# Performance work log

Hardware: AMD Instinct MI355X
Metric: run time of the kernel (lower is better)

Reference implementation:

```python
import jax, jax.numpy as jnp
import numpy as np

B, T, H, STEPS = 8192, 128, 128, 30
BN_EPS = 1e-5


def gru_cell(x, h, w_ih, w_hh, b_ih, b_hh):
    # PyTorch GRU gate math: gates ordered (r, z, n)
    gi = x @ w_ih.T + b_ih            # [B, 3H]
    gh = h @ w_hh.T + b_hh            # [B, 3H]
    ir, iz, inn = jnp.split(gi, 3, axis=-1)
    hr, hz, hn = jnp.split(gh, 3, axis=-1)
    r = jax.nn.sigmoid(ir + hr)
    z = jax.nn.sigmoid(iz + hz)
    n = jnp.tanh(inn + r * hn)
    return (1.0 - z) * n + z * h


def setup_inputs() -> dict:
    key = jax.random.key(0)
    ks = jax.random.split(key, 10)
    s = lambda k, shape: jax.random.normal(k, shape, jnp.float32) * 0.05
    z = lambda *shape: jnp.zeros(shape, jnp.float32)
    return {
        "past": jax.random.normal(ks[0], (B, 6, T), jnp.float32),
        "conv_w": s(ks[1], (H, 6, 3)),
        "conv_b": z(H),
        "bn_gamma": jnp.ones((1,), jnp.float32),
        "bn_beta": z(1),
        "bn_mean": z(1),
        "bn_var": jnp.ones((1,), jnp.float32),
        "enc_wih": s(ks[2], (3 * H, H)),
        "enc_whh": s(ks[3], (3 * H, H)),
        "enc_bih": z(3 * H),
        "enc_bhh": z(3 * H),
        "dec_wih": s(ks[4], (3 * H, H)),
        "dec_whh": s(ks[5], (3 * H, H)),
        "dec_bih": z(3 * H),
        "dec_bhh": z(3 * H),
        "fc1_w": s(ks[6], (256, H)),
        "fc1_b": z(256),
        "fc2_w": s(ks[7], (64, 256)),
        "fc2_b": z(64),
        "fc3_w": s(ks[8], (6, 64)),
        "fc3_b": z(6),
    }


def reference(past, conv_w, conv_b, bn_gamma, bn_beta, bn_mean, bn_var,
              enc_wih, enc_whh, enc_bih, enc_bhh,
              dec_wih, dec_whh, dec_bih, dec_bhh,
              fc1_w, fc1_b, fc2_w, fc2_b, fc3_w, fc3_b):
    b = past.shape[0]
    # Conv1d(6 -> 128, k=3, pad=1) + ReLU
    y = jax.lax.conv_general_dilated(
        past, conv_w, window_strides=(1,), padding=[(1, 1)],
        dimension_numbers=("NCH", "OIH", "NCH"))
    y = jax.nn.relu(y + conv_b[None, :, None])
    # BatchNorm2d(1) in eval mode: single-channel affine normalization over whole tensor
    y = bn_gamma[0] * (y - bn_mean[0]) * jax.lax.rsqrt(bn_var[0] + BN_EPS) + bn_beta[0]
    # encoder GRU over time: [B,128,T] -> [T,B,128]
    xs = jnp.transpose(y, (2, 0, 1))
    h0 = jnp.zeros((b, H), y.dtype)

    def enc_step(h, x):
        return gru_cell(x, h, enc_wih, enc_whh, enc_bih, enc_bhh), None

    state_past, _ = jax.lax.scan(enc_step, h0, xs)  # [B,128]

    def mlp(h):
        a = jax.nn.relu(h @ fc1_w.T + fc1_b)
        a = a @ fc2_w.T + fc2_b   # no activation between fc2 and fc3 (matches Sequential)
        return a @ fc3_w.T + fc3_b

    # decoder input is state_past at step 0, zeros afterwards
    dec_inputs = jnp.concatenate(
        [state_past[None], jnp.zeros((STEPS - 1, b, H), y.dtype)], axis=0)
    present0 = past[:, :, -1]  # [B,6]

    def dec_step(carry, x):
        h, present = carry
        h = gru_cell(x, h, dec_wih, dec_whh, dec_bih, dec_bhh)
        present = present + mlp(h)
        return (h, present), present

    _, preds = jax.lax.scan(dec_step, (jnp.zeros((b, H), y.dtype), present0), dec_inputs)
    # preds: [30,B,6] -> [B,6,30] (matches prediction.permute(0,2,1))
    return jnp.transpose(preds, (1, 2, 0))
```

## Files before the change

kernel.cpp:

```cpp
#include <hip/hip_runtime.h>

#define DI __device__ __forceinline__

typedef __attribute__((ext_vector_type(8))) short short8;
typedef __attribute__((ext_vector_type(4))) float f32x4;

constexpr int THREADS = 512;
constexpr int ROWS    = 32;
constexpr int NBLK    = 8192 / ROWS;
constexpr int PITCH   = 272;
constexpr int PITCH2  = 528;
constexpr int SPITCH  = 256;

constexpr int O_STAGE = 0;
constexpr int O_PATCH = 98304;
constexpr int O_XALL  = 108544;
constexpr int O_H     = 143360;
constexpr int HBUF    = 8704;
constexpr int O_FC3W  = 160768;
constexpr int LDS_TOTAL = 162304;
constexpr int O_A1D   = 98304;
constexpr int O_A2D   = 115200;

DI unsigned cvtpk2(float lo, float hi){
  unsigned r;
  asm("v_cvt_pk_bf16_f32 %0, %1, %2" : "=v"(r) : "v"(lo), "v"(hi));
  return r;
}
DI unsigned short f2bf(float f){ return (unsigned short)cvtpk2(f, f); }
DI float bf2f(unsigned short u){
  union { unsigned u; float f; } v; v.u = ((unsigned)u) << 16;
  return v.f;
}
DI float u2f_lo(unsigned u){ union { unsigned u; float f; } v; v.u = u << 16;        return v.f; }
DI float u2f_hi(unsigned u){ union { unsigned u; float f; } v; v.u = u & 0xffff0000u; return v.f; }
DI float sigm(float x){ return __builtin_amdgcn_rcpf(1.f + __expf(-x)); }
DI float tanh_(float x){ return 2.f * __builtin_amdgcn_rcpf(1.f + __expf(-2.f * x)) - 1.f; }
DI f32x4 mfma16(short8 a, short8 b, f32x4 c){
  return __builtin_amdgcn_mfma_f32_16x16x32_bf16(a, b, c, 0, 0, 0);
}
DI uint2 pack4(f32x4 v){
  return make_uint2(cvtpk2(v[0], v[1]), cvtpk2(v[2], v[3]));
}
DI f32x4 unpack4(uint2 u){
  return (f32x4){u2f_lo(u.x), u2f_hi(u.x), u2f_lo(u.y), u2f_hi(u.y)};
}

DI void stage_k128(char* dst, const float* __restrict__ src, int nrows, int tid){
  const int total = nrows * 32;
  for (int i = tid; i < total; i += THREADS){
    float4 v = ((const float4*)src)[i];
    int e = i << 2;
    int n = e >> 7, k = e & 127;
    *(uint2*)(dst + n * SPITCH + k * 2) = make_uint2(cvtpk2(v.x, v.y), cvtpk2(v.z, v.w));
  }
}
DI void stage_k256(char* dst, const float* __restrict__ src, int nrows, int tid){
  const int total = nrows * 64;
  for (int i = tid; i < total; i += THREADS){
    float4 v = ((const float4*)src)[i];
    int e = i << 2;
    int n = e >> 8, k = e & 255;
    *(uint2*)(dst + n * PITCH2 + k * 2) = make_uint2(cvtpk2(v.x, v.y), cvtpk2(v.z, v.w));
  }
}

__global__ void __launch_bounds__(THREADS, 2)
gru_fused(const float* __restrict__ past,
          const float* __restrict__ conv_w, const float* __restrict__ conv_b,
          const float* __restrict__ bn_gamma, const float* __restrict__ bn_beta,
          const float* __restrict__ bn_mean, const float* __restrict__ bn_var,
          const float* __restrict__ enc_wih, const float* __restrict__ enc_whh,
          const float* __restrict__ enc_bih, const float* __restrict__ enc_bhh,
          const float* __restrict__ dec_wih, const float* __restrict__ dec_whh,
          const float* __restrict__ dec_bih, const float* __restrict__ dec_bhh,
          const float* __restrict__ fc1_w, const float* __restrict__ fc1_b,
          const float* __restrict__ fc2_w, const float* __restrict__ fc2_b,
          const float* __restrict__ fc3_w, const float* __restrict__ fc3_b,
          float* __restrict__ out)
{
  extern __shared__ char smem[];
  const int tid  = threadIdx.x;
  const int lane = tid & 63, w = tid >> 6;
  const int l15  = lane & 15, quad = lane >> 4;
  const int b0   = blockIdx.x * ROWS;
  const int col  = w * 16 + l15;

  const float br_e  = enc_bih[col]       + enc_bhh[col];
  const float bz_e  = enc_bih[128 + col] + enc_bhh[128 + col];
  const float bin_e = enc_bih[256 + col];
  const float bhn_e = enc_bhh[256 + col];
  const float br_d  = dec_bih[col]       + dec_bhh[col];
  const float bz_d  = dec_bih[128 + col] + dec_bhh[128 + col];
  const float bin_d = dec_bih[256 + col];
  const float bhn_d = dec_bhh[256 + col];
  const float cb_t  = conv_b[col];
  const float s_bn  = bn_gamma[0] * rsqrtf(bn_var[0] + 1e-5f);
  const float o_bn  = bn_beta[0] - bn_mean[0] * s_bn;
  const float fb1a  = fc1_b[w * 32 + l15];
  const float fb1b  = fc1_b[w * 32 + 16 + l15];
  const int   mt2   = w & 1, nt2 = w >> 1;
  const float fb2   = fc2_b[nt2 * 16 + l15];

  for (int i = tid; i < 2*HBUF/4; i += THREADS) ((unsigned*)(smem + O_H))[i] = 0u;

  short8 wf[3][4], wh[3][4];
  stage_k128(smem + O_STAGE, enc_wih, 384, tid);
  __syncthreads();
  #pragma unroll
  for (int g = 0; g < 3; ++g)
    #pragma unroll
    for (int kt = 0; kt < 4; ++kt)
      wf[g][kt] = *(const short8*)(smem + O_STAGE + (g*128 + col)*SPITCH + kt*64 + quad*16);
  __syncthreads();
  stage_k128(smem + O_STAGE, enc_whh, 384, tid);
  __syncthreads();
  #pragma unroll
  for (int g = 0; g < 3; ++g)
    #pragma unroll
    for (int kt = 0; kt < 4; ++kt)
      wh[g][kt] = *(const short8*)(smem + O_STAGE + (g*128 + col)*SPITCH + kt*64 + quad*16);
  __syncthreads();

  for (int i = tid; i < 2560; i += THREADS) ((unsigned*)(smem + O_STAGE))[i] = 0u;
  __syncthreads();
  for (int i = tid; i < 2304; i += THREADS){
    int oc = i / 18, kk = i - oc * 18;
    *(unsigned short*)(smem + O_STAGE + oc*80 + kk*2) = f2bf(conv_w[i]);
  }
  __syncthreads();
  const short8 cwf = *(const short8*)(smem + O_STAGE + col*80 + quad*16);
  __syncthreads();

  for (int i = tid; i < 12672; i += THREADS) ((unsigned*)(smem + O_STAGE))[i] = 0u;
  __syncthreads();
  for (int i4 = tid; i4 < 6144; i4 += THREADS){
    int m = i4 / 192, rem = i4 - m*192, c = rem >> 5, t4 = (rem & 31) << 2;
    float4 v = *(const float4*)(past + (size_t)(b0 + m)*768 + c*128 + t4);
    unsigned short* dst = (unsigned short*)(smem + O_STAGE + ((m*6 + c)*132 + t4 + 1)*2);
    dst[0] = f2bf(v.x); dst[1] = f2bf(v.y); dst[2] = f2bf(v.z); dst[3] = f2bf(v.w);
  }
  for (int i = tid; i < 384; i += THREADS) ((float*)(smem + O_FC3W))[i] = fc3_w[i];
  __syncthreads();

  const int e0 = tid;
  const int m0 = e0 / 18, r0 = e0 - m0*18, c0 = r0 / 3, k0 = r0 - c0*3;
  const int e1 = tid + 512;
  const int m1 = e1 / 18, r1 = e1 - m1*18, c1 = r1 / 3, k1 = r1 - c1*3;

  auto patch_entry = [&](int t0, int m, int r18, int c, int k){
    int base = (m*6 + c)*132 + t0 + k;
    const unsigned* pl = (const unsigned*)(smem + O_STAGE);
    unsigned w0 = pl[base >> 1], w1 = pl[(base >> 1) + 1], w2 = pl[(base >> 1) + 2];
    int sh = (base & 1) * 16;
    unsigned long long lo = (unsigned long long)w0 | ((unsigned long long)w1 << 32);
    unsigned long long hi = (unsigned long long)w1 | ((unsigned long long)w2 << 32);
    unsigned a01 = (unsigned)(lo >> sh);
    unsigned a23 = (unsigned)(hi >> sh);
    char* pb = smem + O_PATCH + m*80 + r18*2;
    *(unsigned short*)(pb)          = (unsigned short)(a01 & 0xffff);
    *(unsigned short*)(pb + 2560)   = (unsigned short)(a01 >> 16);
    *(unsigned short*)(pb + 5120)   = (unsigned short)(a23 & 0xffff);
    *(unsigned short*)(pb + 7680)   = (unsigned short)(a23 >> 16);
  };

  uint2 gi_pk[4][2][3];
  float hreg[8];
  #pragma unroll
  for (int i = 0; i < 8; ++i) hreg[i] = 0.f;

  for (int chunk = 0; chunk < 32; ++chunk){
    const int t0 = chunk * 4;
    patch_entry(t0, m0, r0, c0, k0);
    if (e1 < 576) patch_entry(t0, m1, r1, c1, k1);
    __syncthreads();
    #pragma unroll
    for (int mt8 = 0; mt8 < 8; ++mt8){
      short8 pa = *(const short8*)(smem + O_PATCH + (mt8*16 + l15)*80 + quad*16);
      f32x4 cc = (f32x4){0.f,0.f,0.f,0.f};
      cc = mfma16(pa, cwf, cc);
      #pragma unroll
      for (int r = 0; r < 4; ++r){
        int mrow = mt8*16 + quad*4 + r;
        float vx = s_bn * fmaxf(cc[r] + cb_t, 0.f) + o_bn;
        *(unsigned short*)(smem + O_XALL + mrow*PITCH + col*2) = f2bf(vx);
      }
    }
    __syncthreads();
    #pragma unroll
    for (int tc = 0; tc < 4; ++tc)
      #pragma unroll
      for (int mt = 0; mt < 2; ++mt){
        short8 a[4];
        #pragma unroll
        for (int kt = 0; kt < 4; ++kt)
          a[kt] = *(const short8*)(smem + O_XALL + ((tc*2 + mt)*16 + l15)*PITCH + kt*64 + quad*16);
        f32x4 g0 = (f32x4){0.f,0.f,0.f,0.f}, g1 = g0, g2 = g0;
        #pragma unroll
        for (int kt = 0; kt < 4; ++kt){
          g0 = mfma16(a[kt], wf[0][kt], g0);
          g1 = mfma16(a[kt], wf[1][kt], g1);
          g2 = mfma16(a[kt], wf[2][kt], g2);
        }
        gi_pk[tc][mt][0] = pack4(g0);
        gi_pk[tc][mt][1] = pack4(g1);
        gi_pk[tc][mt][2] = pack4(g2);
      }

    #pragma unroll
    for (int tc = 0; tc < 4; ++tc){
      const int t = t0 + tc;
      const char* hr = smem + O_H + (t & 1) * HBUF;
      char*       hw = smem + O_H + ((t + 1) & 1) * HBUF;
      f32x4 accr[2], accz[2], accn2[2], gin[2];
      #pragma unroll
      for (int mt = 0; mt < 2; ++mt){
        accr[mt]  = unpack4(gi_pk[tc][mt][0]);
        accz[mt]  = unpack4(gi_pk[tc][mt][1]);
        gin[mt]   = unpack4(gi_pk[tc][mt][2]);
        accn2[mt] = (f32x4){0.f,0.f,0.f,0.f};
      }
      short8 ha[2][4];
      #pragma unroll
      for (int mt = 0; mt < 2; ++mt)
        #pragma unroll
        for (int kt = 0; kt < 4; ++kt)
          ha[mt][kt] = *(const short8*)(hr + (mt*16 + l15)*PITCH + kt*64 + quad*16);
      #pragma unroll
      for (int mt = 0; mt < 2; ++mt)
        #pragma unroll
        for (int kt = 0; kt < 4; ++kt){
          accr[mt]  = mfma16(ha[mt][kt], wh[0][kt], accr[mt]);
          accz[mt]  = mfma16(ha[mt][kt], wh[1][kt], accz[mt]);
          accn2[mt] = mfma16(ha[mt][kt], wh[2][kt], accn2[mt]);
        }
      #pragma unroll
      for (int mt = 0; mt < 2; ++mt)
        #pragma unroll
        for (int r = 0; r < 4; ++r){
          float rg = sigm(accr[mt][r] + br_e);
          float zg = sigm(accz[mt][r] + bz_e);
          float ng = tanh_(gin[mt][r] + bin_e + rg*(accn2[mt][r] + bhn_e));
          hreg[mt*4 + r] = ng + zg*(hreg[mt*4 + r] - ng);
        }
      #pragma unroll
      for (int mt = 0; mt < 2; ++mt)
        #pragma unroll
        for (int r = 0; r < 4; ++r)
          *(unsigned short*)(hw + (mt*16 + quad*4 + r)*PITCH + col*2) = f2bf(hreg[mt*4 + r]);
      __syncthreads();
    }
  }

  stage_k128(smem + O_STAGE, dec_wih, 384, tid);
  __syncthreads();
  #pragma unroll
  for (int g = 0; g < 3; ++g)
    #pragma unroll
    for (int kt = 0; kt < 4; ++kt)
      wf[g][kt] = *(const short8*)(smem + O_STAGE + (g*128 + col)*SPITCH + kt*64 + quad*16);
  f32x4 gi0r[2], gi0z[2], gi0n[2];
  {
    short8 hea[2][4];
    #pragma unroll
    for (int mt = 0; mt < 2; ++mt)
      #pragma unroll
      for (int kt = 0; kt < 4; ++kt)
        hea[mt][kt] = *(const short8*)(smem + O_H + (mt*16 + l15)*PITCH + kt*64 + quad*16);
    #pragma unroll
    for (int mt = 0; mt < 2; ++mt){
      gi0r[mt] = (f32x4){0.f,0.f,0.f,0.f}; gi0z[mt] = gi0r[mt]; gi0n[mt] = gi0r[mt];
      #pragma unroll
      for (int kt = 0; kt < 4; ++kt){
        gi0r[mt] = mfma16(hea[mt][kt], wf[0][kt], gi0r[mt]);
        gi0z[mt] = mfma16(hea[mt][kt], wf[1][kt], gi0z[mt]);
        gi0n[mt] = mfma16(hea[mt][kt], wf[2][kt], gi0n[mt]);
      }
    }
  }
  __syncthreads();
  stage_k128(smem + O_STAGE, dec_whh, 384, tid);
  __syncthreads();
  #pragma unroll
  for (int g = 0; g < 3; ++g)
    #pragma unroll
    for (int kt = 0; kt < 4; ++kt)
      wh[g][kt] = *(const short8*)(smem + O_STAGE + (g*128 + col)*SPITCH + kt*64 + quad*16);
  __syncthreads();
  short8 f1f[2][4], f2f[8];
  stage_k128(smem + O_STAGE, fc1_w, 256, tid);
  __syncthreads();
  #pragma unroll
  for (int j = 0; j < 2; ++j)
    #pragma unroll
    for (int kt = 0; kt < 4; ++kt)
      f1f[j][kt] = *(const short8*)(smem + O_STAGE + (w*32 + j*16 + l15)*SPITCH + kt*64 + quad*16);
  __syncthreads();
  stage_k256(smem + O_STAGE, fc2_w, 64, tid);
  __syncthreads();
  #pragma unroll
  for (int kt = 0; kt < 8; ++kt)
    f2f[kt] = *(const short8*)(smem + O_STAGE + (nt2*16 + l15)*PITCH2 + kt*64 + quad*16);
  __syncthreads();
  for (int i = tid; i < HBUF/4; i += THREADS) ((unsigned*)(smem + O_H + HBUF))[i] = 0u;
  #pragma unroll
  for (int i = 0; i < 8; ++i) hreg[i] = 0.f;
  const int prow = tid / 6, pcol = tid - prow*6;
  float present = 0.f, fb3 = 0.f;
  if (tid < 192){
    present = past[(size_t)(b0 + prow)*768 + pcol*128 + 127];
    fb3 = fc3_b[pcol];
  }
  __syncthreads();

  for (int s = 0; s < 30; ++s){
    const char* hr = smem + O_H + (1 - (s & 1)) * HBUF;
    char*       hw = smem + O_H + (s & 1) * HBUF;
    f32x4 accr[2], accz[2], accn2[2], gin[2];
    #pragma unroll
    for (int mt = 0; mt < 2; ++mt){
      if (s == 0){ accr[mt] = gi0r[mt]; accz[mt] = gi0z[mt]; gin[mt] = gi0n[mt]; }
      else       { accr[mt] = (f32x4){0.f,0.f,0.f,0.f}; accz[mt] = accr[mt]; gin[mt] = accr[mt]; }
      accn2[mt] = (f32x4){0.f,0.f,0.f,0.f};
    }
    {
      short8 ha[2][4];
      #pragma unroll
      for (int mt = 0; mt < 2; ++mt)
        #pragma unroll
        for (int kt = 0; kt < 4; ++kt)
          ha[mt][kt] = *(const short8*)(hr + (mt*16 + l15)*PITCH + kt*64 + quad*16);
      #pragma unroll
      for (int mt = 0; mt < 2; ++mt)
        #pragma unroll
        for (int kt = 0; kt < 4; ++kt){
          accr[mt]  = mfma16(ha[mt][kt], wh[0][kt], accr[mt]);
          accz[mt]  = mfma16(ha[mt][kt], wh[1][kt], accz[mt]);
          accn2[mt] = mfma16(ha[mt][kt], wh[2][kt], accn2[mt]);
        }
    }
    #pragma unroll
    for (int mt = 0; mt < 2; ++mt)
      #pragma unroll
      for (int r = 0; r < 4; ++r){
        float rg = sigm(accr[mt][r] + br_d);
        float zg = sigm(accz[mt][r] + bz_d);
        float ng = tanh_(gin[mt][r] + bin_d + rg*(accn2[mt][r] + bhn_d));
        hreg[mt*4 + r] = ng + zg*(hreg[mt*4 + r] - ng);
      }
    #pragma unroll
    for (int mt = 0; mt < 2; ++mt)
      #pragma unroll
      for (int r = 0; r < 4; ++r)
        *(unsigned short*)(hw + (mt*16 + quad*4 + r)*PITCH + col*2) = f2bf(hreg[mt*4 + r]);
    __syncthreads();

    {
      short8 hf[2][4];
      #pragma unroll
      for (int mt = 0; mt < 2; ++mt)
        #pragma unroll
        for (int kt = 0; kt < 4; ++kt)
          hf[mt][kt] = *(const short8*)(hw + (mt*16 + l15)*PITCH + kt*64 + quad*16);
      f32x4 a1a[2][2];
      #pragma unroll
      for (int mt = 0; mt < 2; ++mt)
        #pragma unroll
        for (int j = 0; j < 2; ++j) a1a[mt][j] = (f32x4){0.f,0.f,0.f,0.f};
      #pragma unroll
      for (int j = 0; j < 2; ++j)
        #pragma unroll
        for (int kt = 0; kt < 4; ++kt){
          a1a[0][j] = mfma16(hf[0][kt], f1f[j][kt], a1a[0][j]);
          a1a[1][j] = mfma16(hf[1][kt], f1f[j][kt], a1a[1][j]);
        }
      #pragma unroll
      for (int mt = 0; mt < 2; ++mt)
        #pragma unroll
        for (int j = 0; j < 2; ++j){
          float bb = j ? fb1b : fb1a;
          #pragma unroll
          for (int r = 0; r < 4; ++r)
            *(unsigned short*)(smem + O_A1D + (mt*16 + quad*4 + r)*PITCH2 +
                               (w*32 + j*16 + l15)*2) = f2bf(fmaxf(a1a[mt][j][r] + bb, 0.f));
        }
    }
    __syncthreads();

    {
      f32x4 a2a = (f32x4){0.f,0.f,0.f,0.f};
      #pragma unroll
      for (int kt = 0; kt < 8; ++kt){
        short8 a = *(const short8*)(smem + O_A1D + (mt2*16 + l15)*PITCH2 + kt*64 + quad*16);
        a2a = mfma16(a, f2f[kt], a2a);
      }
      #pragma unroll
      for (int r = 0; r < 4; ++r)
        *(unsigned short*)(smem + O_A2D + (mt2*16 + quad*4 + r)*144 + (nt2*16 + l15)*2) =
            f2bf(a2a[r] + fb2);
    }
    __syncthreads();

    if (tid < 192){
      float o = fb3;
      const float* w3 = (const float*)(smem + O_FC3W) + pcol*64;
      #pragma unroll
      for (int kc = 0; kc < 8; ++kc){
        short8 av = *(const short8*)(smem + O_A2D + prow*144 + kc*16);
        #pragma unroll
        for (int j = 0; j < 8; ++j)
          o += bf2f((unsigned short)av[j]) * w3[kc*8 + j];
      }
      present += o;
      out[(size_t)(b0 + prow)*180 + pcol*30 + s] = present;
    }
  }
}

extern "C" void kernel_launch(void* const* d_in, const int* in_sizes, int n_in,
                              void* d_out, int out_size, void* d_ws, size_t ws_size,
                              hipStream_t stream) {
  (void)in_sizes; (void)n_in; (void)out_size; (void)d_ws; (void)ws_size;
  const float* past     = (const float*)d_in[0];
  const float* conv_w   = (const float*)d_in[1];
  const float* conv_b   = (const float*)d_in[2];
  const float* bn_gamma = (const float*)d_in[3];
  const float* bn_beta  = (const float*)d_in[4];
  const float* bn_mean  = (const float*)d_in[5];
  const float* bn_var   = (const float*)d_in[6];
  const float* enc_wih  = (const float*)d_in[7];
  const float* enc_whh  = (const float*)d_in[8];
  const float* enc_bih  = (const float*)d_in[9];
  const float* enc_bhh  = (const float*)d_in[10];
  const float* dec_wih  = (const float*)d_in[11];
  const float* dec_whh  = (const float*)d_in[12];
  const float* dec_bih  = (const float*)d_in[13];
  const float* dec_bhh  = (const float*)d_in[14];
  const float* fc1_w    = (const float*)d_in[15];
  const float* fc1_b    = (const float*)d_in[16];
  const float* fc2_w    = (const float*)d_in[17];
  const float* fc2_b    = (const float*)d_in[18];
  const float* fc3_w    = (const float*)d_in[19];
  const float* fc3_b    = (const float*)d_in[20];

  hipFuncSetAttribute((const void*)gru_fused,
                      hipFuncAttributeMaxDynamicSharedMemorySize, LDS_TOTAL);

  gru_fused<<<NBLK, THREADS, LDS_TOTAL, stream>>>(
      past, conv_w, conv_b, bn_gamma, bn_beta, bn_mean, bn_var,
      enc_wih, enc_whh, enc_bih, enc_bhh,
      dec_wih, dec_whh, dec_bih, dec_bhh,
      fc1_w, fc1_b, fc2_w, fc2_b, fc3_w, fc3_b,
      (float*)d_out);
}
```

Before: 498.4 us.

## Halve rows per block and shrink LDS to allow four blocks per CU

Cuts the batch rows handled per workgroup from 32 to 16, which doubles the grid and halves the per-block LDS footprint (weights are now staged one gate at a time). Launch bounds move to four blocks per CU so more blocks can be resident at once and hide the serial GRU step latency. In exchange each block issues half as many MFMAs per barrier, the fc2 stage leaves half the waves idle, and register pressure must fit the tighter launch bound.

```diff
diff --git a/kernel.cpp b/kernel.cpp
--- a/kernel.cpp
+++ b/kernel.cpp
@@ -6,21 +6,22 @@
 typedef __attribute__((ext_vector_type(4))) float f32x4;
 
 constexpr int THREADS = 512;
-constexpr int ROWS    = 32;
+constexpr int ROWS    = 16;
 constexpr int NBLK    = 8192 / ROWS;
 constexpr int PITCH   = 272;
 constexpr int PITCH2  = 528;
 constexpr int SPITCH  = 256;
 
+constexpr int O_PAST  = 0;
+constexpr int O_PATCH = 25344;
+constexpr int O_XALL  = 30464;
+constexpr int O_H     = 47872;
+constexpr int HBUF    = 4352;
+constexpr int O_FC3W  = 56576;
+constexpr int LDS_TOTAL = 58112;
 constexpr int O_STAGE = 0;
-constexpr int O_PATCH = 98304;
-constexpr int O_XALL  = 108544;
-constexpr int O_H     = 143360;
-constexpr int HBUF    = 8704;
-constexpr int O_FC3W  = 160768;
-constexpr int LDS_TOTAL = 162304;
-constexpr int O_A1D   = 98304;
-constexpr int O_A2D   = 115200;
+constexpr int O_A1D   = 25344;
+constexpr int O_A2D   = 33792;
 
 DI unsigned cvtpk2(float lo, float hi){
   unsigned r;
@@ -65,7 +66,7 @@
   }
 }
 
-__global__ void __launch_bounds__(THREADS, 2)
+__global__ void __launch_bounds__(THREADS, 4)
 gru_fused(const float* __restrict__ past,
           const float* __restrict__ conv_w, const float* __restrict__ conv_b,
           const float* __restrict__ bn_gamma, const float* __restrict__ bn_beta,
@@ -99,28 +100,29 @@
   const float o_bn  = bn_beta[0] - bn_mean[0] * s_bn;
   const float fb1a  = fc1_b[w * 32 + l15];
   const float fb1b  = fc1_b[w * 32 + 16 + l15];
-  const int   mt2   = w & 1, nt2 = w >> 1;
-  const float fb2   = fc2_b[nt2 * 16 + l15];
+  const float fb2   = fc2_b[(w & 3) * 16 + l15];
 
   for (int i = tid; i < 2*HBUF/4; i += THREADS) ((unsigned*)(smem + O_H))[i] = 0u;
 
   short8 wf[3][4], wh[3][4];
-  stage_k128(smem + O_STAGE, enc_wih, 384, tid);
-  __syncthreads();
-  #pragma unroll
-  for (int g = 0; g < 3; ++g)
+  #pragma unroll
+  for (int g = 0; g < 3; ++g){
+    stage_k128(smem + O_STAGE, enc_wih + g*16384, 128, tid);
+    __syncthreads();
     #pragma unroll
     for (int kt = 0; kt < 4; ++kt)
-      wf[g][kt] = *(const short8*)(smem + O_STAGE + (g*128 + col)*SPITCH + kt*64 + quad*16);
-  __syncthreads();
-  stage_k128(smem + O_STAGE, enc_whh, 384, tid);
-  __syncthreads();
-  #pragma unroll
-  for (int g = 0; g < 3; ++g)
+      wf[g][kt] = *(const short8*)(smem + O_STAGE + col*SPITCH + kt*64 + quad*16);
+    __syncthreads();
+  }
+  #pragma unroll
+  for (int g = 0; g < 3; ++g){
+    stage_k128(smem + O_STAGE, enc_whh + g*16384, 128, tid);
+    __syncthreads();
     #pragma unroll
     for (int kt = 0; kt < 4; ++kt)
-      wh[g][kt] = *(const short8*)(smem + O_STAGE + (g*128 + col)*SPITCH + kt*64 + quad*16);
-  __syncthreads();
+      wh[g][kt] = *(const short8*)(smem + O_STAGE + col*SPITCH + kt*64 + quad*16);
+    __syncthreads();
+  }
 
   for (int i = tid; i < 2560; i += THREADS) ((unsigned*)(smem + O_STAGE))[i] = 0u;
   __syncthreads();
@@ -132,12 +134,12 @@
   const short8 cwf = *(const short8*)(smem + O_STAGE + col*80 + quad*16);
   __syncthreads();
 
-  for (int i = tid; i < 12672; i += THREADS) ((unsigned*)(smem + O_STAGE))[i] = 0u;
-  __syncthreads();
-  for (int i4 = tid; i4 < 6144; i4 += THREADS){
+  for (int i = tid; i < 6336; i += THREADS) ((unsigned*)(smem + O_PAST))[i] = 0u;
+  __syncthreads();
+  for (int i4 = tid; i4 < 3072; i4 += THREADS){
     int m = i4 / 192, rem = i4 - m*192, c = rem >> 5, t4 = (rem & 31) << 2;
     float4 v = *(const float4*)(past + (size_t)(b0 + m)*768 + c*128 + t4);
-    unsigned short* dst = (unsigned short*)(smem + O_STAGE + ((m*6 + c)*132 + t4 + 1)*2);
+    unsigned short* dst = (unsigned short*)(smem + O_PAST + ((m*6 + c)*132 + t4 + 1)*2);
     dst[0] = f2bf(v.x); dst[1] = f2bf(v.y); dst[2] = f2bf(v.z); dst[3] = f2bf(v.w);
   }
   for (int i = tid; i < 384; i += THREADS) ((float*)(smem + O_FC3W))[i] = fc3_w[i];
@@ -145,12 +147,10 @@
 
   const int e0 = tid;
   const int m0 = e0 / 18, r0 = e0 - m0*18, c0 = r0 / 3, k0 = r0 - c0*3;
-  const int e1 = tid + 512;
-  const int m1 = e1 / 18, r1 = e1 - m1*18, c1 = r1 / 3, k1 = r1 - c1*3;
 
   auto patch_entry = [&](int t0, int m, int r18, int c, int k){
     int base = (m*6 + c)*132 + t0 + k;
-    const unsigned* pl = (const unsigned*)(smem + O_STAGE);
+    const unsigned* pl = (const unsigned*)(smem + O_PAST);
     unsigned w0 = pl[base >> 1], w1 = pl[(base >> 1) + 1], w2 = pl[(base >> 1) + 2];
     int sh = (base & 1) * 16;
     unsigned long long lo = (unsigned long long)w0 | ((unsigned long long)w1 << 32);
@@ -159,23 +159,22 @@
     unsigned a23 = (unsigned)(hi >> sh);
     char* pb = smem + O_PATCH + m*80 + r18*2;
     *(unsigned short*)(pb)          = (unsigned short)(a01 & 0xffff);
-    *(unsigned short*)(pb + 2560)   = (unsigned short)(a01 >> 16);
-    *(unsigned short*)(pb + 5120)   = (unsigned short)(a23 & 0xffff);
-    *(unsigned short*)(pb + 7680)   = (unsigned short)(a23 >> 16);
+    *(unsigned short*)(pb + 1280)   = (unsigned short)(a01 >> 16);
+    *(unsigned short*)(pb + 2560)   = (unsigned short)(a23 & 0xffff);
+    *(unsigned short*)(pb + 3840)   = (unsigned short)(a23 >> 16);
   };
 
-  uint2 gi_pk[4][2][3];
-  float hreg[8];
-  #pragma unroll
-  for (int i = 0; i < 8; ++i) hreg[i] = 0.f;
+  uint2 gi_pk[4][3];
+  float hreg[4];
+  #pragma unroll
+  for (int i = 0; i < 4; ++i) hreg[i] = 0.f;
 
   for (int chunk = 0; chunk < 32; ++chunk){
     const int t0 = chunk * 4;
-    patch_entry(t0, m0, r0, c0, k0);
-    if (e1 < 576) patch_entry(t0, m1, r1, c1, k1);
-    __syncthreads();
-    #pragma unroll
-    for (int mt8 = 0; mt8 < 8; ++mt8){
+    if (e0 < 288) patch_entry(t0, m0, r0, c0, k0);
+    __syncthreads();
+    #pragma unroll
+    for (int mt8 = 0; mt8 < 4; ++mt8){
       short8 pa = *(const short8*)(smem + O_PATCH + (mt8*16 + l15)*80 + quad*16);
       f32x4 cc = (f32x4){0.f,0.f,0.f,0.f};
       cc = mfma16(pa, cwf, cc);
@@ -188,126 +187,122 @@
     }
     __syncthreads();
     #pragma unroll
-    for (int tc = 0; tc < 4; ++tc)
-      #pragma unroll
-      for (int mt = 0; mt < 2; ++mt){
-        short8 a[4];
-        #pragma unroll
-        for (int kt = 0; kt < 4; ++kt)
-          a[kt] = *(const short8*)(smem + O_XALL + ((tc*2 + mt)*16 + l15)*PITCH + kt*64 + quad*16);
-        f32x4 g0 = (f32x4){0.f,0.f,0.f,0.f}, g1 = g0, g2 = g0;
-        #pragma unroll
-        for (int kt = 0; kt < 4; ++kt){
-          g0 = mfma16(a[kt], wf[0][kt], g0);
-          g1 = mfma16(a[kt], wf[1][kt], g1);
-          g2 = mfma16(a[kt], wf[2][kt], g2);
-        }
-        gi_pk[tc][mt][0] = pack4(g0);
-        gi_pk[tc][mt][1] = pack4(g1);
-        gi_pk[tc][mt][2] = pack4(g2);
-      }
+    for (int tc = 0; tc < 4; ++tc){
+      short8 a[4];
+      #pragma unroll
+      for (int kt = 0; kt < 4; ++kt)
+        a[kt] = *(const short8*)(smem + O_XALL + (tc*16 + l15)*PITCH + kt*64 + quad*16);
+      f32x4 g0 = (f32x4){0.f,0.f,0.f,0.f}, g1 = g0, g2 = g0;
+      #pragma unroll
+      for (int kt = 0; kt < 4; ++kt){
+        g0 = mfma16(a[kt], wf[0][kt], g0);
+        g1 = mfma16(a[kt], wf[1][kt], g1);
+        g2 = mfma16(a[kt], wf[2][kt], g2);
+      }
+      gi_pk[tc][0] = pack4(g0);
+      gi_pk[tc][1] = pack4(g1);
+      gi_pk[tc][2] = pack4(g2);
+    }
 
     #pragma unroll
     for (int tc = 0; tc < 4; ++tc){
       const int t = t0 + tc;
       const char* hr = smem + O_H + (t & 1) * HBUF;
       char*       hw = smem + O_H + ((t + 1) & 1) * HBUF;
-      f32x4 accr[2], accz[2], accn2[2], gin[2];
-      #pragma unroll
-      for (int mt = 0; mt < 2; ++mt){
-        accr[mt]  = unpack4(gi_pk[tc][mt][0]);
-        accz[mt]  = unpack4(gi_pk[tc][mt][1]);
-        gin[mt]   = unpack4(gi_pk[tc][mt][2]);
-        accn2[mt] = (f32x4){0.f,0.f,0.f,0.f};
-      }
-      short8 ha[2][4];
-      #pragma unroll
-      for (int mt = 0; mt < 2; ++mt)
-        #pragma unroll
-        for (int kt = 0; kt < 4; ++kt)
-          ha[mt][kt] = *(const short8*)(hr + (mt*16 + l15)*PITCH + kt*64 + quad*16);
-      #pragma unroll
-      for (int mt = 0; mt < 2; ++mt)
-        #pragma unroll
-        for (int kt = 0; kt < 4; ++kt){
-          accr[mt]  = mfma16(ha[mt][kt], wh[0][kt], accr[mt]);
-          accz[mt]  = mfma16(ha[mt][kt], wh[1][kt], accz[mt]);
-          accn2[mt] = mfma16(ha[mt][kt], wh[2][kt], accn2[mt]);
-        }
-      #pragma unroll
-      for (int mt = 0; mt < 2; ++mt)
-        #pragma unroll
-        for (int r = 0; r < 4; ++r){
-          float rg = sigm(accr[mt][r] + br_e);
-          float zg = sigm(accz[mt][r] + bz_e);
-          float ng = tanh_(gin[mt][r] + bin_e + rg*(accn2[mt][r] + bhn_e));
-          hreg[mt*4 + r] = ng + zg*(hreg[mt*4 + r] - ng);
-        }
-      #pragma unroll
-      for (int mt = 0; mt < 2; ++mt)
-        #pragma unroll
-        for (int r = 0; r < 4; ++r)
-          *(unsigned short*)(hw + (mt*16 + quad*4 + r)*PITCH + col*2) = f2bf(hreg[mt*4 + r]);
+      f32x4 accr = unpack4(gi_pk[tc][0]);
+      f32x4 accz = unpack4(gi_pk[tc][1]);
+      f32x4 gin  = unpack4(gi_pk[tc][2]);
+      f32x4 accn2 = (f32x4){0.f,0.f,0.f,0.f};
+      short8 ha[4];
+      #pragma unroll
+      for (int kt = 0; kt < 4; ++kt)
+        ha[kt] = *(const short8*)(hr + l15*PITCH + kt*64 + quad*16);
+      #pragma unroll
+      for (int kt = 0; kt < 4; ++kt){
+        accr  = mfma16(ha[kt], wh[0][kt], accr);
+        accz  = mfma16(ha[kt], wh[1][kt], accz);
+        accn2 = mfma16(ha[kt], wh[2][kt], accn2);
+      }
+      #pragma unroll
+      for (int r = 0; r < 4; ++r){
+        float rg = sigm(accr[r] + br_e);
+        float zg = sigm(accz[r] + bz_e);
+        float ng = tanh_(gin[r] + bin_e + rg*(accn2[r] + bhn_e));
+        hreg[r] = ng + zg*(hreg[r] - ng);
+      }
+      #pragma unroll
+      for (int r = 0; r < 4; ++r)
+        *(unsigned short*)(hw + (quad*4 + r)*PITCH + col*2) = f2bf(hreg[r]);
       __syncthreads();
     }
   }
 
-  stage_k128(smem + O_STAGE, dec_wih, 384, tid);
-  __syncthreads();
-  #pragma unroll
-  for (int g = 0; g < 3; ++g)
+  #pragma unroll
+  for (int g = 0; g < 3; ++g){
+    stage_k128(smem + O_STAGE, dec_wih + g*16384, 128, tid);
+    __syncthreads();
     #pragma unroll
     for (int kt = 0; kt < 4; ++kt)
-      wf[g][kt] = *(const short8*)(smem + O_STAGE + (g*128 + col)*SPITCH + kt*64 + quad*16);
-  f32x4 gi0r[2], gi0z[2], gi0n[2];
+      wf[g][kt] = *(const short8*)(smem + O_STAGE + col*SPITCH + kt*64 + quad*16);
+    __syncthreads();
+  }
+  f32x4 gi0r, gi0z, gi0n;
   {
-    short8 hea[2][4];
-    #pragma unroll
-    for (int mt = 0; mt < 2; ++mt)
-      #pragma unroll
-      for (int kt = 0; kt < 4; ++kt)
-        hea[mt][kt] = *(const short8*)(smem + O_H + (mt*16 + l15)*PITCH + kt*64 + quad*16);
-    #pragma unroll
-    for (int mt = 0; mt < 2; ++mt){
-      gi0r[mt] = (f32x4){0.f,0.f,0.f,0.f}; gi0z[mt] = gi0r[mt]; gi0n[mt] = gi0r[mt];
-      #pragma unroll
-      for (int kt = 0; kt < 4; ++kt){
-        gi0r[mt] = mfma16(hea[mt][kt], wf[0][kt], gi0r[mt]);
-        gi0z[mt] = mfma16(hea[mt][kt], wf[1][kt], gi0z[mt]);
-        gi0n[mt] = mfma16(hea[mt][kt], wf[2][kt], gi0n[mt]);
-      }
-    }
-  }
-  __syncthreads();
-  stage_k128(smem + O_STAGE, dec_whh, 384, tid);
-  __syncthreads();
-  #pragma unroll
-  for (int g = 0; g < 3; ++g)
+    short8 hea[4];
     #pragma unroll
     for (int kt = 0; kt < 4; ++kt)
-      wh[g][kt] = *(const short8*)(smem + O_STAGE + (g*128 + col)*SPITCH + kt*64 + quad*16);
-  __syncthreads();
+      hea[kt] = *(const short8*)(smem + O_H + l15*PITCH + kt*64 + quad*16);
+    gi0r = (f32x4){0.f,0.f,0.f,0.f}; gi0z = gi0r; gi0n = gi0r;
+    #pragma unroll
+    for (int kt = 0; kt < 4; ++kt){
+      gi0r = mfma16(hea[kt], wf[0][kt], gi0r);
+      gi0z = mfma16(hea[kt], wf[1][kt], gi0z);
+      gi0n = mfma16(hea[kt], wf[2][kt], gi0n);
+    }
+  }
+  __syncthreads();
+  #pragma unroll
+  for (int g = 0; g < 3; ++g){
+    stage_k128(smem + O_STAGE, dec_whh + g*16384, 128, tid);
+    __syncthreads();
+    #pragma unroll
+    for (int kt = 0; kt < 4; ++kt)
+      wh[g][kt] = *(const short8*)(smem + O_STAGE + col*SPITCH + kt*64 + quad*16);
+    __syncthreads();
+  }
   short8 f1f[2][4], f2f[8];
-  stage_k128(smem + O_STAGE, fc1_w, 256, tid);
-  __syncthreads();
-  #pragma unroll
-  for (int j = 0; j < 2; ++j)
-    #pragma unroll
-    for (int kt = 0; kt < 4; ++kt)
-      f1f[j][kt] = *(const short8*)(smem + O_STAGE + (w*32 + j*16 + l15)*SPITCH + kt*64 + quad*16);
+  stage_k128(smem + O_STAGE, fc1_w, 128, tid);
+  __syncthreads();
+  if (w < 4){
+    #pragma unroll
+    for (int j = 0; j < 2; ++j)
+      #pragma unroll
+      for (int kt = 0; kt < 4; ++kt)
+        f1f[j][kt] = *(const short8*)(smem + O_STAGE + (w*32 + j*16 + l15)*SPITCH + kt*64 + quad*16);
+  }
+  __syncthreads();
+  stage_k128(smem + O_STAGE, fc1_w + 16384, 128, tid);
+  __syncthreads();
+  if (w >= 4){
+    #pragma unroll
+    for (int j = 0; j < 2; ++j)
+      #pragma unroll
+      for (int kt = 0; kt < 4; ++kt)
+        f1f[j][kt] = *(const short8*)(smem + O_STAGE + ((w-4)*32 + j*16 + l15)*SPITCH + kt*64 + quad*16);
+  }
   __syncthreads();
   stage_k256(smem + O_STAGE, fc2_w, 64, tid);
   __syncthreads();
   #pragma unroll
   for (int kt = 0; kt < 8; ++kt)
-    f2f[kt] = *(const short8*)(smem + O_STAGE + (nt2*16 + l15)*PITCH2 + kt*64 + quad*16);
+    f2f[kt] = *(const short8*)(smem + O_STAGE + ((w & 3)*16 + l15)*PITCH2 + kt*64 + quad*16);
   __syncthreads();
   for (int i = tid; i < HBUF/4; i += THREADS) ((unsigned*)(smem + O_H + HBUF))[i] = 0u;
   #pragma unroll
-  for (int i = 0; i < 8; ++i) hreg[i] = 0.f;
+  for (int i = 0; i < 4; ++i) hreg[i] = 0.f;
   const int prow = tid / 6, pcol = tid - prow*6;
   float present = 0.f, fb3 = 0.f;
-  if (tid < 192){
+  if (tid < 96){
     present = past[(size_t)(b0 + prow)*768 + pcol*128 + 127];
     fb3 = fc3_b[pcol];
   }
@@ -316,92 +311,73 @@
   for (int s = 0; s < 30; ++s){
     const char* hr = smem + O_H + (1 - (s & 1)) * HBUF;
     char*       hw = smem + O_H + (s & 1) * HBUF;
-    f32x4 accr[2], accz[2], accn2[2], gin[2];
-    #pragma unroll
-    for (int mt = 0; mt < 2; ++mt){
-      if (s == 0){ accr[mt] = gi0r[mt]; accz[mt] = gi0z[mt]; gin[mt] = gi0n[mt]; }
-      else       { accr[mt] = (f32x4){0.f,0.f,0.f,0.f}; accz[mt] = accr[mt]; gin[mt] = accr[mt]; }
-      accn2[mt] = (f32x4){0.f,0.f,0.f,0.f};
-    }
+    f32x4 accr, accz, gin;
+    if (s == 0){ accr = gi0r; accz = gi0z; gin = gi0n; }
+    else       { accr = (f32x4){0.f,0.f,0.f,0.f}; accz = accr; gin = accr; }
+    f32x4 accn2 = (f32x4){0.f,0.f,0.f,0.f};
     {
-      short8 ha[2][4];
-      #pragma unroll
-      for (int mt = 0; mt < 2; ++mt)
+      short8 ha[4];
+      #pragma unroll
+      for (int kt = 0; kt < 4; ++kt)
+        ha[kt] = *(const short8*)(hr + l15*PITCH + kt*64 + quad*16);
+      #pragma unroll
+      for (int kt = 0; kt < 4; ++kt){
+        accr  = mfma16(ha[kt], wh[0][kt], accr);
+        accz  = mfma16(ha[kt], wh[1][kt], accz);
+        accn2 = mfma16(ha[kt], wh[2][kt], accn2);
+      }
+    }
+    #pragma unroll
+    for (int r = 0; r < 4; ++r){
+      float rg = sigm(accr[r] + br_d);
+      float zg = sigm(accz[r] + bz_d);
+      float ng = tanh_(gin[r] + bin_d + rg*(accn2[r] + bhn_d));
+      hreg[r] = ng + zg*(hreg[r] - ng);
+    }
+    #pragma unroll
+    for (int r = 0; r < 4; ++r)
+      *(unsigned short*)(hw + (quad*4 + r)*PITCH + col*2) = f2bf(hreg[r]);
+    __syncthreads();
+
+    {
+      short8 hf[4];
+      #pragma unroll
+      for (int kt = 0; kt < 4; ++kt)
+        hf[kt] = *(const short8*)(hw + l15*PITCH + kt*64 + quad*16);
+      f32x4 a1a[2];
+      #pragma unroll
+      for (int j = 0; j < 2; ++j) a1a[j] = (f32x4){0.f,0.f,0.f,0.f};
+      #pragma unroll
+      for (int j = 0; j < 2; ++j)
         #pragma unroll
         for (int kt = 0; kt < 4; ++kt)
-          ha[mt][kt] = *(const short8*)(hr + (mt*16 + l15)*PITCH + kt*64 + quad*16);
-      #pragma unroll
-      for (int mt = 0; mt < 2; ++mt)
+          a1a[j] = mfma16(hf[kt], f1f[j][kt], a1a[j]);
+      #pragma unroll
+      for (int j = 0; j < 2; ++j){
+        float bb = j ? fb1b : fb1a;
         #pragma unroll
-        for (int kt = 0; kt < 4; ++kt){
-          accr[mt]  = mfma16(ha[mt][kt], wh[0][kt], accr[mt]);
-          accz[mt]  = mfma16(ha[mt][kt], wh[1][kt], accz[mt]);
-          accn2[mt] = mfma16(ha[mt][kt], wh[2][kt], accn2[mt]);
-        }
-    }
-    #pragma unroll
-    for (int mt = 0; mt < 2; ++mt)
-      #pragma unroll
-      for (int r = 0; r < 4; ++r){
-        float rg = sigm(accr[mt][r] + br_d);
-        float zg = sigm(accz[mt][r] + bz_d);
-        float ng = tanh_(gin[mt][r] + bin_d + rg*(accn2[mt][r] + bhn_d));
-        hreg[mt*4 + r] = ng + zg*(hreg[mt*4 + r] - ng);
-      }
-    #pragma unroll
-    for (int mt = 0; mt < 2; ++mt)
+        for (int r = 0; r < 4; ++r)
+          *(unsigned short*)(smem + O_A1D + (quad*4 + r)*PITCH2 +
+                             (w*32 + j*16 + l15)*2) = f2bf(fmaxf(a1a[j][r] + bb, 0.f));
+      }
+    }
+    __syncthreads();
+
+    if (w < 4){
+      f32x4 a2a = (f32x4){0.f,0.f,0.f,0.f};
+      #pragma unroll
+      for (int kt = 0; kt < 8; ++kt){
+        short8 a = *(const short8*)(smem + O_A1D + l15*PITCH2 + kt*64 + quad*16);
+        a2a = mfma16(a, f2f[kt], a2a);
+      }
       #pragma unroll
       for (int r = 0; r < 4; ++r)
-        *(unsigned short*)(hw + (mt*16 + quad*4 + r)*PITCH + col*2) = f2bf(hreg[mt*4 + r]);
-    __syncthreads();
-
-    {
-      short8 hf[2][4];
-      #pragma unroll
-      for (int mt = 0; mt < 2; ++mt)
-        #pragma unroll
-        for (int kt = 0; kt < 4; ++kt)
-          hf[mt][kt] = *(const short8*)(hw + (mt*16 + l15)*PITCH + kt*64 + quad*16);
-      f32x4 a1a[2][2];
-      #pragma unroll
-      for (int mt = 0; mt < 2; ++mt)
-        #pragma unroll
-        for (int j = 0; j < 2; ++j) a1a[mt][j] = (f32x4){0.f,0.f,0.f,0.f};
-      #pragma unroll
-      for (int j = 0; j < 2; ++j)
-        #pragma unroll
-        for (int kt = 0; kt < 4; ++kt){
-          a1a[0][j] = mfma16(hf[0][kt], f1f[j][kt], a1a[0][j]);
-          a1a[1][j] = mfma16(hf[1][kt], f1f[j][kt], a1a[1][j]);
-        }
-      #pragma unroll
-      for (int mt = 0; mt < 2; ++mt)
-        #pragma unroll
-        for (int j = 0; j < 2; ++j){
-          float bb = j ? fb1b : fb1a;
-          #pragma unroll
-          for (int r = 0; r < 4; ++r)
-            *(unsigned short*)(smem + O_A1D + (mt*16 + quad*4 + r)*PITCH2 +
-                               (w*32 + j*16 + l15)*2) = f2bf(fmaxf(a1a[mt][j][r] + bb, 0.f));
-        }
-    }
-    __syncthreads();
-
-    {
-      f32x4 a2a = (f32x4){0.f,0.f,0.f,0.f};
-      #pragma unroll
-      for (int kt = 0; kt < 8; ++kt){
-        short8 a = *(const short8*)(smem + O_A1D + (mt2*16 + l15)*PITCH2 + kt*64 + quad*16);
-        a2a = mfma16(a, f2f[kt], a2a);
-      }
-      #pragma unroll
-      for (int r = 0; r < 4; ++r)
-        *(unsigned short*)(smem + O_A2D + (mt2*16 + quad*4 + r)*144 + (nt2*16 + l15)*2) =
+        *(unsigned short*)(smem + O_A2D + (quad*4 + r)*144 + (w*16 + l15)*2) =
             f2bf(a2a[r] + fb2);
     }
     __syncthreads();
 
-    if (tid < 192){
+    if (tid < 96){
       float o = fb3;
       const float* w3 = (const float*)(smem + O_FC3W) + pcol*64;
       #pragma unroll
```

Measured after the change: 784.4 us. +57.4%, slower.

## Software-pipeline conv and input projection for next chunk into encoder GRU steps

Applied to the files above, without the earlier changes.

The encoder loop is restructured so that the conv and input-gate GEMM for chunk c+1 are interleaved with the four recurrent GRU steps of chunk c, with a prologue that fills the first chunk. The independent MFMA work can then hide latency in the serial hidden-state chain, and the barriers per chunk drop from six to four. The cost is more live registers, since gi_pk is now overwritten while still in use, and a more intricate ordering between the patch, XALL and gi buffers, which could hurt occupancy or scheduling.

```diff
diff --git a/kernel.cpp b/kernel.cpp
--- a/kernel.cpp
+++ b/kernel.cpp
@@ -163,17 +163,17 @@
     *(unsigned short*)(pb + 5120)   = (unsigned short)(a23 & 0xffff);
     *(unsigned short*)(pb + 7680)   = (unsigned short)(a23 >> 16);
   };
+  auto patchA1 = [&](int t0){
+    patch_entry(t0, m0, r0, c0, k0);
+    if (e1 < 576) patch_entry(t0, m1, r1, c1, k1);
+  };
 
   uint2 gi_pk[4][2][3];
   float hreg[8];
   #pragma unroll
   for (int i = 0; i < 8; ++i) hreg[i] = 0.f;
 
-  for (int chunk = 0; chunk < 32; ++chunk){
-    const int t0 = chunk * 4;
-    patch_entry(t0, m0, r0, c0, k0);
-    if (e1 < 576) patch_entry(t0, m1, r1, c1, k1);
-    __syncthreads();
+  auto conv_block = [&](){
     #pragma unroll
     for (int mt8 = 0; mt8 < 8; ++mt8){
       short8 pa = *(const short8*)(smem + O_PATCH + (mt8*16 + l15)*80 + quad*16);
@@ -186,70 +186,89 @@
         *(unsigned short*)(smem + O_XALL + mrow*PITCH + col*2) = f2bf(vx);
       }
     }
-    __syncthreads();
-    #pragma unroll
-    for (int tc = 0; tc < 4; ++tc)
-      #pragma unroll
-      for (int mt = 0; mt < 2; ++mt){
-        short8 a[4];
-        #pragma unroll
-        for (int kt = 0; kt < 4; ++kt)
-          a[kt] = *(const short8*)(smem + O_XALL + ((tc*2 + mt)*16 + l15)*PITCH + kt*64 + quad*16);
-        f32x4 g0 = (f32x4){0.f,0.f,0.f,0.f}, g1 = g0, g2 = g0;
-        #pragma unroll
-        for (int kt = 0; kt < 4; ++kt){
-          g0 = mfma16(a[kt], wf[0][kt], g0);
-          g1 = mfma16(a[kt], wf[1][kt], g1);
-          g2 = mfma16(a[kt], wf[2][kt], g2);
-        }
-        gi_pk[tc][mt][0] = pack4(g0);
-        gi_pk[tc][mt][1] = pack4(g1);
-        gi_pk[tc][mt][2] = pack4(g2);
-      }
-
-    #pragma unroll
-    for (int tc = 0; tc < 4; ++tc){
-      const int t = t0 + tc;
-      const char* hr = smem + O_H + (t & 1) * HBUF;
-      char*       hw = smem + O_H + ((t + 1) & 1) * HBUF;
-      f32x4 accr[2], accz[2], accn2[2], gin[2];
-      #pragma unroll
-      for (int mt = 0; mt < 2; ++mt){
-        accr[mt]  = unpack4(gi_pk[tc][mt][0]);
-        accz[mt]  = unpack4(gi_pk[tc][mt][1]);
-        gin[mt]   = unpack4(gi_pk[tc][mt][2]);
-        accn2[mt] = (f32x4){0.f,0.f,0.f,0.f};
-      }
-      short8 ha[2][4];
-      #pragma unroll
-      for (int mt = 0; mt < 2; ++mt)
-        #pragma unroll
-        for (int kt = 0; kt < 4; ++kt)
-          ha[mt][kt] = *(const short8*)(hr + (mt*16 + l15)*PITCH + kt*64 + quad*16);
-      #pragma unroll
-      for (int mt = 0; mt < 2; ++mt)
-        #pragma unroll
-        for (int kt = 0; kt < 4; ++kt){
-          accr[mt]  = mfma16(ha[mt][kt], wh[0][kt], accr[mt]);
-          accz[mt]  = mfma16(ha[mt][kt], wh[1][kt], accz[mt]);
-          accn2[mt] = mfma16(ha[mt][kt], wh[2][kt], accn2[mt]);
-        }
-      #pragma unroll
-      for (int mt = 0; mt < 2; ++mt)
-        #pragma unroll
-        for (int r = 0; r < 4; ++r){
-          float rg = sigm(accr[mt][r] + br_e);
-          float zg = sigm(accz[mt][r] + bz_e);
-          float ng = tanh_(gin[mt][r] + bin_e + rg*(accn2[mt][r] + bhn_e));
-          hreg[mt*4 + r] = ng + zg*(hreg[mt*4 + r] - ng);
-        }
-      #pragma unroll
-      for (int mt = 0; mt < 2; ++mt)
-        #pragma unroll
-        for (int r = 0; r < 4; ++r)
-          *(unsigned short*)(hw + (mt*16 + quad*4 + r)*PITCH + col*2) = f2bf(hreg[mt*4 + r]);
-      __syncthreads();
-    }
+  };
+  auto gi_unit = [&](int tc, int mt){
+    short8 a[4];
+    #pragma unroll
+    for (int kt = 0; kt < 4; ++kt)
+      a[kt] = *(const short8*)(smem + O_XALL + ((tc*2 + mt)*16 + l15)*PITCH + kt*64 + quad*16);
+    f32x4 g0 = (f32x4){0.f,0.f,0.f,0.f}, g1 = g0, g2 = g0;
+    #pragma unroll
+    for (int kt = 0; kt < 4; ++kt){
+      g0 = mfma16(a[kt], wf[0][kt], g0);
+      g1 = mfma16(a[kt], wf[1][kt], g1);
+      g2 = mfma16(a[kt], wf[2][kt], g2);
+    }
+    gi_pk[tc][mt][0] = pack4(g0);
+    gi_pk[tc][mt][1] = pack4(g1);
+    gi_pk[tc][mt][2] = pack4(g2);
+  };
+  auto step_body = [&](int t){
+    const int tc = t & 3;
+    const char* hr = smem + O_H + (t & 1) * HBUF;
+    char*       hw = smem + O_H + ((t + 1) & 1) * HBUF;
+    f32x4 accr[2], accz[2], accn2[2], gin[2];
+    #pragma unroll
+    for (int mt = 0; mt < 2; ++mt){
+      accr[mt]  = unpack4(gi_pk[tc][mt][0]);
+      accz[mt]  = unpack4(gi_pk[tc][mt][1]);
+      gin[mt]   = unpack4(gi_pk[tc][mt][2]);
+      accn2[mt] = (f32x4){0.f,0.f,0.f,0.f};
+    }
+    short8 ha[2][4];
+    #pragma unroll
+    for (int mt = 0; mt < 2; ++mt)
+      #pragma unroll
+      for (int kt = 0; kt < 4; ++kt)
+        ha[mt][kt] = *(const short8*)(hr + (mt*16 + l15)*PITCH + kt*64 + quad*16);
+    #pragma unroll
+    for (int mt = 0; mt < 2; ++mt)
+      #pragma unroll
+      for (int kt = 0; kt < 4; ++kt){
+        accr[mt]  = mfma16(ha[mt][kt], wh[0][kt], accr[mt]);
+        accz[mt]  = mfma16(ha[mt][kt], wh[1][kt], accz[mt]);
+        accn2[mt] = mfma16(ha[mt][kt], wh[2][kt], accn2[mt]);
+      }
+    #pragma unroll
+    for (int mt = 0; mt < 2; ++mt)
+      #pragma unroll
+      for (int r = 0; r < 4; ++r){
+        float rg = sigm(accr[mt][r] + br_e);
+        float zg = sigm(accz[mt][r] + bz_e);
+        float ng = tanh_(gin[mt][r] + bin_e + rg*(accn2[mt][r] + bhn_e));
+        hreg[mt*4 + r] = ng + zg*(hreg[mt*4 + r] - ng);
+      }
+    #pragma unroll
+    for (int mt = 0; mt < 2; ++mt)
+      #pragma unroll
+      for (int r = 0; r < 4; ++r)
+        *(unsigned short*)(hw + (mt*16 + quad*4 + r)*PITCH + col*2) = f2bf(hreg[mt*4 + r]);
+  };
+
+  patchA1(0);
+  __syncthreads();
+  conv_block();
+  __syncthreads();
+  #pragma unroll
+  for (int tc = 0; tc < 4; ++tc){ gi_unit(tc, 0); gi_unit(tc, 1); }
+  patchA1(4);
+  __syncthreads();
+
+  for (int c = 0; c < 32; ++c){
+    const int t0 = c * 4;
+    const bool prod = (c < 31);
+    step_body(t0 + 0);
+    if (prod) conv_block();
+    __syncthreads();
+    step_body(t0 + 1);
+    if (prod){ gi_unit(0,0); gi_unit(0,1); gi_unit(1,0); }
+    __syncthreads();
+    step_body(t0 + 2);
+    if (prod){ gi_unit(1,1); gi_unit(2,0); gi_unit(2,1); }
+    __syncthreads();
+    step_body(t0 + 3);
+    if (prod){ gi_unit(3,0); gi_unit(3,1); if (c < 30) patchA1(t0 + 8); }
+    __syncthreads();
   }
 
   stage_k128(smem + O_STAGE, dec_wih, 384, tid);
```

Result: faster. 471.9 us (-5.3%).
